# Kernel tuning notes

Hardware: AMD Instinct MI355X
Metric: run time of the kernel (lower is better)

Reference implementation:

```python
import jax, jax.numpy as jnp
import numpy as np

B, S, D = 8, 1024, 1024
E, M, K = 8, 4096, 2
GROUP = 1024
CAP = int(np.ceil(GROUP * K / E))  # 256 tokens per expert per group


def setup_inputs() -> dict:
    key = jax.random.key(0)
    ks = jax.random.split(key, 4)
    x = jax.random.normal(ks[0], (B, S, D), dtype=jnp.float32)
    w_router = jax.random.normal(ks[1], (D, E), dtype=jnp.float32) * 0.02
    w1 = jax.random.normal(ks[2], (E, D, M), dtype=jnp.float32) * (1.0 / np.sqrt(D))
    b1 = jnp.zeros((E, M), dtype=jnp.float32)
    w2 = jax.random.normal(ks[3], (E, M, D), dtype=jnp.float32) * (1.0 / np.sqrt(M))
    b2 = jnp.zeros((E, D), dtype=jnp.float32)
    return {"x": x, "w_router": w_router, "w1": w1, "b1": b1, "w2": w2, "b2": b2}


def _moe_forward(x, w_router, w1, b1, w2, b2):
    # Group tokens: [G, GROUP, D]
    xg = x.reshape(-1, GROUP, D)
    G = xg.shape[0]
    # Router: gates over experts per token.
    logits = jnp.einsum('gsd,de->gse', xg, w_router)
    gates = jax.nn.softmax(logits, axis=-1)  # [G, S, E]
    topk_vals, topk_idx = jax.lax.top_k(gates, K)  # [G, S, K]
    oh = jax.nn.one_hot(topk_idx, E, dtype=xg.dtype)  # [G, S, K, E]

    # Position in each expert's buffer: choice-0 of all tokens has priority
    # over choice-1 (standard top-k MoE priority ordering).
    prev = jnp.zeros((G, 1, E), dtype=xg.dtype)
    dispatch = jnp.zeros((G, GROUP, E, CAP), dtype=xg.dtype)
    combine = jnp.zeros((G, GROUP, E, CAP), dtype=xg.dtype)
    for k in range(K):
        ohk = oh[:, :, k, :]                                  # [G, S, E]
        csum = jnp.cumsum(ohk, axis=1) - ohk + prev           # slots used before this token
        pos_k = jnp.sum(csum * ohk, axis=-1)                  # [G, S]
        keep = (pos_k < CAP).astype(xg.dtype)
        pos_oh = jax.nn.one_hot(pos_k, CAP, dtype=xg.dtype)   # [G, S, C]
        d_k = ohk[:, :, :, None] * pos_oh[:, :, None, :] * keep[:, :, None, None]
        dispatch = dispatch + d_k
        combine = combine + topk_vals[:, :, k, None, None] * d_k
        prev = prev + jnp.sum(ohk, axis=1, keepdims=True)

    # Dispatch tokens into per-expert buffers: [E, G, C, D]
    xe = jnp.einsum('gsec,gsd->egcd', dispatch, xg)
    # Per-expert MLP (gelu, approximate=True as in flax Dense MlpBlock).
    h = jax.nn.gelu(jnp.einsum('egcd,edm->egcm', xe, w1) + b1[:, None, None, :])
    ye = jnp.einsum('egcm,emd->egcd', h, w2) + b2[:, None, None, :]
    # Combine back to tokens, weighted by gates.
    out = jnp.einsum('gsec,egcd->gsd', combine, ye)
    out = out.reshape(B, S, D)

    # Importance auxiliary metric (squared coefficient of variation of gate mass).
    imp = jnp.sum(gates, axis=1)  # [G, E]
    aux = jnp.mean((jnp.std(imp, axis=-1) / jnp.mean(imp, axis=-1)) ** 2)
    return out, aux


def reference(x, w_router, w1, b1, w2, b2):
    return _moe_forward(x, w_router, w1, b1, w2, b2)
```

## Files before the change

kernel.cpp:

```cpp
#include <hip/hip_runtime.h>

#define D_DIM 1024
#define E_EXP 8
#define M_DIM 4096
#define N_GRP 8
#define GRP_SZ 1024
#define CAPACITY 256
#define N_TOK (N_GRP * GRP_SZ)
#define SLOT_ROWS (E_EXP * N_GRP * CAPACITY)
#define ROWS_PER_E (N_GRP * CAPACITY)

typedef _Float16 half8_t __attribute__((ext_vector_type(8)));
typedef float f32x4_t __attribute__((ext_vector_type(4)));

__device__ __forceinline__ void async_copy16(void* lds, const void* gptr) {
  __builtin_amdgcn_global_load_lds(
      (__attribute__((address_space(1))) void*)(void*)(const_cast<void*>(gptr)),
      (__attribute__((address_space(3))) void*)lds,
      16, 0, 0);
}

__device__ __forceinline__ float fast_gelu(float v) {
  float w2 = 1.5957691216057308f * (v + 0.044715f * v * v * v);
  float ex = __expf(w2);
  float t = 1.0f - 2.0f * __builtin_amdgcn_rcpf(1.0f + ex);
  return 0.5f * v * (1.0f + t);
}

__global__ __launch_bounds__(256)
void router_kernel(const float* __restrict__ x, const float* __restrict__ wr,
                   float* __restrict__ gates, int* __restrict__ tk_idx,
                   float* __restrict__ tk_val) {
  __shared__ __attribute__((aligned(16))) float wrT[E_EXP * D_DIM];
  const int tid = threadIdx.x;
  for (int i = tid; i < E_EXP * D_DIM; i += 256) {
    int d = i >> 3, e = i & 7;
    wrT[e * D_DIM + d] = wr[i];
  }
  __syncthreads();
  const int wv = tid >> 6, lane = tid & 63;
  const int token = blockIdx.x * 4 + wv;
  const float4* xr = (const float4*)(x + (size_t)token * D_DIM);
  float lg[8] = {0.f, 0.f, 0.f, 0.f, 0.f, 0.f, 0.f, 0.f};
#pragma unroll
  for (int it = 0; it < 4; it++) {
    float4 v = xr[it * 64 + lane];
#pragma unroll
    for (int e = 0; e < 8; e++) {
      float4 w = *(const float4*)&wrT[e * D_DIM + (it * 64 + lane) * 4];
      lg[e] += v.x * w.x + v.y * w.y + v.z * w.z + v.w * w.w;
    }
  }
#pragma unroll
  for (int off = 32; off > 0; off >>= 1) {
#pragma unroll
    for (int e = 0; e < 8; e++) lg[e] += __shfl_xor(lg[e], off, 64);
  }
  if (lane == 0) {
    float mx = lg[0];
#pragma unroll
    for (int e = 1; e < 8; e++) mx = fmaxf(mx, lg[e]);
    float s = 0.f, g[8];
#pragma unroll
    for (int e = 0; e < 8; e++) { g[e] = expf(lg[e] - mx); s += g[e]; }
    float inv = 1.0f / s;
#pragma unroll
    for (int e = 0; e < 8; e++) { g[e] *= inv; gates[(size_t)token * 8 + e] = g[e]; }
    int i0 = 0; float v0 = g[0];
    for (int e = 1; e < 8; e++) if (g[e] > v0) { v0 = g[e]; i0 = e; }
    int i1 = -1; float v1 = -1.f;
    for (int e = 0; e < 8; e++) if (e != i0 && g[e] > v1) { v1 = g[e]; i1 = e; }
    tk_idx[token * 2 + 0] = i0; tk_idx[token * 2 + 1] = i1;
    tk_val[token * 2 + 0] = v0; tk_val[token * 2 + 1] = v1;
  }
}

__global__ void scan_kernel(const int* __restrict__ tk_idx,
                            int* __restrict__ slot_src,
                            int* __restrict__ assign_row) {
  const int g = blockIdx.x;
  const int lane = threadIdx.x;
  const unsigned long long below = (1ull << lane) - 1ull;
  int ev[32];
#pragma unroll
  for (int k = 0; k < 2; k++)
#pragma unroll
    for (int ch = 0; ch < 16; ch++)
      ev[k * 16 + ch] = tk_idx[((size_t)g * GRP_SZ + ch * 64 + lane) * 2 + k];
  int cnt[8] = {0, 0, 0, 0, 0, 0, 0, 0};
#pragma unroll
  for (int k = 0; k < 2; k++) {
#pragma unroll
    for (int ch = 0; ch < 16; ch++) {
      const int s = ch * 64 + lane;
      const int e = ev[k * 16 + ch];
      int pos = 0;
#pragma unroll
      for (int ee = 0; ee < 8; ee++) {
        unsigned long long m = __ballot(e == ee);
        if (e == ee) pos = cnt[ee] + (int)__popcll(m & below);
        cnt[ee] += (int)__popcll(m);
      }
      int row = (pos < CAPACITY) ? ((e * N_GRP + g) * CAPACITY + pos) : -1;
      assign_row[((size_t)g * GRP_SZ + s) * 2 + k] = row;
      if (row >= 0) slot_src[row] = s;
    }
  }
  for (int e = 0; e < 8; e++)
    for (int c = lane; c < CAPACITY; c += 64)
      if (c >= cnt[e]) slot_src[(e * N_GRP + g) * CAPACITY + c] = -1;
}

__global__ __launch_bounds__(256)
void gather_kernel(const float* __restrict__ x, const int* __restrict__ slot_src,
                   _Float16* __restrict__ A1) {
  const int row = blockIdx.x;
  const int g = (row >> 8) & 7;
  const int t = threadIdx.x;
  const int s = slot_src[row];
  float2* dst = (float2*)(A1 + (size_t)row * D_DIM);
  if (s < 0) { dst[t] = make_float2(0.f, 0.f); return; }
  const float4 v = ((const float4*)x)[((size_t)g * GRP_SZ + s) * (D_DIM / 4) + t];
  union { _Float16 h[4]; float2 f2; } u;
  u.h[0] = (_Float16)v.x; u.h[1] = (_Float16)v.y;
  u.h[2] = (_Float16)v.z; u.h[3] = (_Float16)v.w;
  dst[t] = u.f2;
}

__global__ __launch_bounds__(256)
void transpose_both_kernel(const float* __restrict__ w1, const float* __restrict__ w2,
                           _Float16* __restrict__ w1t, _Float16* __restrict__ w2t) {
  __shared__ float tile[32][33];
  const int z = blockIdx.y;
  const float* sp;
  _Float16* dp;
  int R, C;
  if (z < 8) { sp = w1 + (size_t)z * D_DIM * M_DIM; dp = w1t + (size_t)z * D_DIM * M_DIM; R = D_DIM; C = M_DIM; }
  else       { sp = w2 + (size_t)(z - 8) * M_DIM * D_DIM; dp = w2t + (size_t)(z - 8) * M_DIM * D_DIM; R = M_DIM; C = D_DIM; }
  const int tiles_x = C >> 5;
  const int c0 = (blockIdx.x % tiles_x) * 32, r0 = (blockIdx.x / tiles_x) * 32;
  {
    const int row = threadIdx.x >> 3;
    const int cb = (threadIdx.x & 7) * 4;
    float4 v = *(const float4*)&sp[(size_t)(r0 + row) * C + c0 + cb];
    tile[row][cb + 0] = v.x; tile[row][cb + 1] = v.y;
    tile[row][cb + 2] = v.z; tile[row][cb + 3] = v.w;
  }
  __syncthreads();
  const int cl = threadIdx.x >> 3;
  const int ch = threadIdx.x & 7;
  union { _Float16 h[4]; float2 f2; } u;
#pragma unroll
  for (int k = 0; k < 4; k++) u.h[k] = (_Float16)tile[ch * 4 + k][cl];
  *(float2*)&dp[(size_t)(c0 + cl) * R + r0 + ch * 4] = u.f2;
}

template <int KDIM, int NDIM, int EPI>
__global__ __launch_bounds__(256)
void gemm_bt_kernel(const _Float16* __restrict__ Aall,
                    const _Float16* __restrict__ BTall,
                    const float* __restrict__ biasAll,
                    void* __restrict__ CoutAll) {
  const int e = blockIdx.z;
  const _Float16* A = Aall + (size_t)e * ROWS_PER_E * KDIM;
  const _Float16* BT = BTall + (size_t)e * NDIM * KDIM;
  const float* bias = biasAll + (size_t)e * NDIM;

  constexpr int NYT = NDIM / 128;
  const int yt = blockIdx.x % NYT;
  const int xt = blockIdx.x / NYT;
  const int rowblk = xt * 128;
  const int colblk = yt * 128;

  const int tid = threadIdx.x;
  const int wave = tid >> 6, lane = tid & 63;
  const int wm = (wave & 1) * 64, wn = (wave >> 1) * 64;

  __shared__ __attribute__((aligned(16))) _Float16 As0[128 * 64];
  __shared__ __attribute__((aligned(16))) _Float16 As1[128 * 64];
  __shared__ __attribute__((aligned(16))) _Float16 Bs0[128 * 64];
  __shared__ __attribute__((aligned(16))) _Float16 Bs1[128 * 64];

  f32x4_t acc[4][4] = {};

  const int l_r = lane >> 3, l_c = lane & 7;
  const _Float16* gA[4];
  const _Float16* gB[4];
  int ldsOff[4];
#pragma unroll
  for (int i = 0; i < 4; i++) {
    const int rbase = i * 32 + wave * 8;
    const int r = rbase + l_r;
    const int q = l_c ^ (r & 7);
    gA[i] = A + (size_t)(rowblk + r) * KDIM + q * 8;
    gB[i] = BT + (size_t)(colblk + r) * KDIM + q * 8;
    ldsOff[i] = rbase * 64;
  }

  const int quad = lane >> 4;
  const int ln = lane & 15;
  int offA[4], offB[4];
#pragma unroll
  for (int i = 0; i < 4; i++) {
    int m = wm + i * 16 + ln;
    offA[i] = m * 64 + (quad ^ (m & 7)) * 8;
    int n = wn + i * 16 + ln;
    offB[i] = n * 64 + (quad ^ (n & 7)) * 8;
  }

  _Float16* curA = As0; _Float16* nxtA = As1;
  _Float16* curB = Bs0; _Float16* nxtB = Bs1;

#pragma unroll
  for (int i = 0; i < 4; i++) async_copy16(curA + ldsOff[i], gA[i]);
#pragma unroll
  for (int i = 0; i < 4; i++) async_copy16(curB + ldsOff[i], gB[i]);

  for (int kt = 0; kt < KDIM; kt += 64) {
    __syncthreads();
    if (kt + 64 < KDIM) {
#pragma unroll
      for (int i = 0; i < 4; i++) async_copy16(nxtA + ldsOff[i], gA[i] + kt + 64);
#pragma unroll
      for (int i = 0; i < 4; i++) async_copy16(nxtB + ldsOff[i], gB[i] + kt + 64);
    }
#pragma unroll
    for (int h = 0; h < 2; h++) {
      half8_t af[4], bf[4];
#pragma unroll
      for (int i = 0; i < 4; i++) {
        af[i] = *(const half8_t*)&curA[offA[i] ^ (h * 32)];
        bf[i] = *(const half8_t*)&curB[offB[i] ^ (h * 32)];
      }
#pragma unroll
      for (int i = 0; i < 4; i++)
#pragma unroll
        for (int j = 0; j < 4; j++)
          acc[i][j] = __builtin_amdgcn_mfma_f32_16x16x32_f16(af[i], bf[j], acc[i][j], 0, 0, 0);
    }
    _Float16* t;
    t = curA; curA = nxtA; nxtA = t;
    t = curB; curB = nxtB; nxtB = t;
  }

  if constexpr (EPI == 1) {
    _Float16* C = (_Float16*)CoutAll + (size_t)e * ROWS_PER_E * NDIM;
#pragma unroll
    for (int p = 0; p < 4; p++) {
      __syncthreads();
      const int lr0 = (wave & 1) * 16 + quad * 4;
#pragma unroll
      for (int j = 0; j < 4; j++) {
        const int col = wn + j * 16 + ln;
        const float bcol = bias[colblk + col];
#pragma unroll
        for (int r = 0; r < 4; r++) {
          float v = acc[p][j][r] + bcol;
          As0[(lr0 + r) * 136 + col] = (_Float16)fast_gelu(v);
        }
      }
      __syncthreads();
#pragma unroll
      for (int q = 0; q < 2; q++) {
        const int lrw = q * 16 + (tid >> 4);
        const int chunk = tid & 15;
        const int gr = (lrw >= 16 ? 64 : 0) + p * 16 + (lrw & 15);
        float4 vv = *(const float4*)&As0[lrw * 136 + chunk * 8];
        *(float4*)&C[(size_t)(rowblk + gr) * NDIM + colblk + chunk * 8] = vv;
      }
    }
  } else {
    float* C = (float*)CoutAll + (size_t)e * ROWS_PER_E * NDIM;
    const int colb = colblk + wn + ln;
    const int rowb = rowblk + wm + quad * 4;
#pragma unroll
    for (int j = 0; j < 4; j++) {
      const int col = colb + j * 16;
      const float bcol = bias[col];
#pragma unroll
      for (int i = 0; i < 4; i++) {
#pragma unroll
        for (int r = 0; r < 4; r++) {
          const int row = rowb + i * 16 + r;
          C[(size_t)row * NDIM + col] = acc[i][j][r] + bcol;
        }
      }
    }
  }
}

__global__ __launch_bounds__(256)
void combine_kernel(const float* __restrict__ ye, const int* __restrict__ assign_row,
                    const float* __restrict__ tk_val, float* __restrict__ out) {
  const int t = blockIdx.x;
  const int d = threadIdx.x;
  const int r0 = assign_row[t * 2 + 0];
  const int r1 = assign_row[t * 2 + 1];
  const float g0 = tk_val[t * 2 + 0];
  const float g1 = tk_val[t * 2 + 1];
  const float4* y4 = (const float4*)ye;
  float4 v = make_float4(0.f, 0.f, 0.f, 0.f);
  if (r0 >= 0) {
    float4 a = y4[(size_t)r0 * (D_DIM / 4) + d];
    v.x += g0 * a.x; v.y += g0 * a.y; v.z += g0 * a.z; v.w += g0 * a.w;
  }
  if (r1 >= 0) {
    float4 a = y4[(size_t)r1 * (D_DIM / 4) + d];
    v.x += g1 * a.x; v.y += g1 * a.y; v.z += g1 * a.z; v.w += g1 * a.w;
  }
  ((float4*)out)[(size_t)t * (D_DIM / 4) + d] = v;
}

__global__ __launch_bounds__(256)
void aux1_kernel(const float* __restrict__ gates, float* __restrict__ imp) {
  const int g = blockIdx.x >> 3, e = blockIdx.x & 7;
  const int tid = threadIdx.x, lane = tid & 63, wave = tid >> 6;
  float s = 0.f;
  for (int t = tid; t < GRP_SZ; t += 256)
    s += gates[((size_t)g * GRP_SZ + t) * 8 + e];
#pragma unroll
  for (int off = 32; off > 0; off >>= 1) s += __shfl_xor(s, off, 64);
  __shared__ float ws4[4];
  if (lane == 0) ws4[wave] = s;
  __syncthreads();
  if (tid == 0) imp[blockIdx.x] = ws4[0] + ws4[1] + ws4[2] + ws4[3];
}

__global__ void aux2_kernel(const float* __restrict__ imp, float* __restrict__ aux_out) {
  const int t = threadIdx.x;
  __shared__ float cvS[8];
  if (t < 8) {
    float mean = 0.f;
    for (int k = 0; k < 8; k++) mean += imp[t * 8 + k];
    mean *= 0.125f;
    float var = 0.f;
    for (int k = 0; k < 8; k++) { float dd = imp[t * 8 + k] - mean; var += dd * dd; }
    var *= 0.125f;
    cvS[t] = var / (mean * mean);
  }
  __syncthreads();
  if (t == 0) {
    float a = 0.f;
    for (int k = 0; k < 8; k++) a += cvS[k];
    aux_out[0] = a * 0.125f;
  }
}

extern "C" void kernel_launch(void* const* d_in, const int* in_sizes, int n_in,
                              void* d_out, int out_size, void* d_ws, size_t ws_size,
                              hipStream_t stream) {
  const float* x  = (const float*)d_in[0];
  const float* wr = (const float*)d_in[1];
  const float* w1 = (const float*)d_in[2];
  const float* b1 = (const float*)d_in[3];
  const float* w2 = (const float*)d_in[4];
  const float* b2 = (const float*)d_in[5];
  float* out = (float*)d_out;

  char* ws = (char*)d_ws;
  size_t off = 0;
  auto alloc = [&](size_t bytes) -> void* {
    void* p = ws + off;
    off += (bytes + 255) & ~(size_t)255;
    return p;
  };
  float*     gates      = (float*)alloc((size_t)N_TOK * 8 * 4);
  int*       tk_idx     = (int*)  alloc((size_t)N_TOK * 2 * 4);
  float*     tk_val     = (float*)alloc((size_t)N_TOK * 2 * 4);
  int*       assign_row = (int*)  alloc((size_t)N_TOK * 2 * 4);
  int*       slot_src   = (int*)  alloc((size_t)SLOT_ROWS * 4);
  float*     imp        = (float*)alloc(64 * 4);
  _Float16*  A1  = (_Float16*)alloc((size_t)SLOT_ROWS * D_DIM * 2);
  _Float16*  w1t = (_Float16*)alloc((size_t)E_EXP * M_DIM * D_DIM * 2);
  _Float16*  w2t = (_Float16*)alloc((size_t)E_EXP * D_DIM * M_DIM * 2);
  _Float16*  H   = (_Float16*)alloc((size_t)SLOT_ROWS * M_DIM * 2);
  float*     ye  = (float*)   alloc((size_t)SLOT_ROWS * D_DIM * 4);
  if (off > ws_size) return;

  router_kernel<<<N_TOK / 4, 256, 0, stream>>>(x, wr, gates, tk_idx, tk_val);
  scan_kernel<<<N_GRP, 64, 0, stream>>>(tk_idx, slot_src, assign_row);
  gather_kernel<<<SLOT_ROWS, 256, 0, stream>>>(x, slot_src, A1);
  transpose_both_kernel<<<dim3(4096, 16), 256, 0, stream>>>(w1, w2, w1t, w2t);
  gemm_bt_kernel<D_DIM, M_DIM, 1><<<dim3((ROWS_PER_E / 128) * (M_DIM / 128), 1, E_EXP), 256, 0, stream>>>(A1, w1t, b1, H);
  gemm_bt_kernel<M_DIM, D_DIM, 2><<<dim3((ROWS_PER_E / 128) * (D_DIM / 128), 1, E_EXP), 256, 0, stream>>>(H, w2t, b2, ye);
  combine_kernel<<<N_TOK, 256, 0, stream>>>(ye, assign_row, tk_val, out);
  aux1_kernel<<<64, 256, 0, stream>>>(gates, imp);
  aux2_kernel<<<1, 64, 0, stream>>>(imp, out + (size_t)N_TOK * D_DIM);
}
```

Before: 747.2 us.

## Replace expert GEMMs with 256x256-tile, 512-thread pipelined MFMA kernel

Rewrites the two per-expert GEMMs to use 256x256 output tiles with 8 waves, each wave computing a 128x64 sub-tile. The new kernel streams K in 32-wide sub-stages through a 128KB double-buffered LDS ring, waits on explicit vmcnt counts, and raises wave priority around MFMA bursts. Block indices are remapped for L2 locality. The goal is more operand reuse per LDS byte and better overlap of global loads with MFMA. In exchange, the dynamic LDS use is large and occupancy drops, the grid has fewer blocks (which may underfill CUs for the second GEMM), and the fragile wait counting raises correctness risk.

```diff
diff --git a/kernel.cpp b/kernel.cpp
--- a/kernel.cpp
+++ b/kernel.cpp
@@ -156,136 +156,153 @@
 }
 
 template <int KDIM, int NDIM, int EPI>
-__global__ __launch_bounds__(256)
-void gemm_bt_kernel(const _Float16* __restrict__ Aall,
+__global__ __launch_bounds__(512, 2)
+void gemm256_kernel(const _Float16* __restrict__ Aall,
                     const _Float16* __restrict__ BTall,
                     const float* __restrict__ biasAll,
                     void* __restrict__ CoutAll) {
+  constexpr int NT = KDIM / 64;
+  constexpr int NXT = ROWS_PER_E / 256;
+  constexpr int NYT = NDIM / 256;
+  constexpr int NB = NXT * NYT;
+  static_assert(NXT == 8 && (NB % 8) == 0 && NT >= 4, "geometry");
+
+  extern __shared__ __attribute__((aligned(16))) _Float16 smem[];
+  _Float16* lA = smem;
+  _Float16* lB = smem + 32768;
+
   const int e = blockIdx.z;
-  const _Float16* A = Aall + (size_t)e * ROWS_PER_E * KDIM;
+  const _Float16* A  = Aall  + (size_t)e * ROWS_PER_E * KDIM;
   const _Float16* BT = BTall + (size_t)e * NDIM * KDIM;
-  const float* bias = biasAll + (size_t)e * NDIM;
-
-  constexpr int NYT = NDIM / 128;
-  const int yt = blockIdx.x % NYT;
-  const int xt = blockIdx.x / NYT;
-  const int rowblk = xt * 128;
-  const int colblk = yt * 128;
+  const float* bias  = biasAll + (size_t)e * NDIM;
+
+  const int bswz = (blockIdx.x & 7) * (NB >> 3) + (blockIdx.x >> 3);
+  const int xt = bswz & (NXT - 1);
+  const int yt = bswz >> 3;
+  const int rowblk = xt * 256;
+  const int colblk = yt * 256;
 
   const int tid = threadIdx.x;
   const int wave = tid >> 6, lane = tid & 63;
-  const int wm = (wave & 1) * 64, wn = (wave >> 1) * 64;
-
-  __shared__ __attribute__((aligned(16))) _Float16 As0[128 * 64];
-  __shared__ __attribute__((aligned(16))) _Float16 As1[128 * 64];
-  __shared__ __attribute__((aligned(16))) _Float16 Bs0[128 * 64];
-  __shared__ __attribute__((aligned(16))) _Float16 Bs1[128 * 64];
-
-  f32x4_t acc[4][4] = {};
-
-  const int l_r = lane >> 3, l_c = lane & 7;
-  const _Float16* gA[4];
-  const _Float16* gB[4];
-  int ldsOff[4];
-#pragma unroll
-  for (int i = 0; i < 4; i++) {
-    const int rbase = i * 32 + wave * 8;
-    const int r = rbase + l_r;
-    const int q = l_c ^ (r & 7);
-    gA[i] = A + (size_t)(rowblk + r) * KDIM + q * 8;
-    gB[i] = BT + (size_t)(colblk + r) * KDIM + q * 8;
-    ldsOff[i] = rbase * 64;
-  }
-
-  const int quad = lane >> 4;
-  const int ln = lane & 15;
-  int offA[4], offB[4];
-#pragma unroll
-  for (int i = 0; i < 4; i++) {
-    int m = wm + i * 16 + ln;
-    offA[i] = m * 64 + (quad ^ (m & 7)) * 8;
-    int n = wn + i * 16 + ln;
-    offB[i] = n * 64 + (quad ^ (n & 7)) * 8;
-  }
-
-  _Float16* curA = As0; _Float16* nxtA = As1;
-  _Float16* curB = Bs0; _Float16* nxtB = Bs1;
-
-#pragma unroll
-  for (int i = 0; i < 4; i++) async_copy16(curA + ldsOff[i], gA[i]);
-#pragma unroll
-  for (int i = 0; i < 4; i++) async_copy16(curB + ldsOff[i], gB[i]);
-
-  for (int kt = 0; kt < KDIM; kt += 64) {
-    __syncthreads();
-    if (kt + 64 < KDIM) {
-#pragma unroll
-      for (int i = 0; i < 4; i++) async_copy16(nxtA + ldsOff[i], gA[i] + kt + 64);
-#pragma unroll
-      for (int i = 0; i < 4; i++) async_copy16(nxtB + ldsOff[i], gB[i] + kt + 64);
+  const int wm = wave >> 2, wn = wave & 3;
+  const int quad = lane >> 4, ln = lane & 15;
+
+  const int schunk = (tid & 7) ^ ((tid >> 3) & 7);
+  const int rowA = ((tid >> 3) << 1) + (schunk >> 2);
+  const int colA = (schunk & 3) << 3;
+  const _Float16* baseA = A  + (size_t)(rowblk + rowA) * KDIM + colA;
+  const _Float16* baseB = BT + (size_t)(colblk + rowA) * KDIM + colA;
+  const int ldsW = wave * 512;
+
+  auto stage_unit = [&](int u) {
+    const int tu = u >> 2;
+    const int j = u & 3;
+    const int ks = j >> 1;
+    const int koff = tu * 64 + ks * 32;
+    const int slot = ((tu & 1) * 2 + ks) * 8192 + ldsW;
+    if ((j & 1) == 0) {
+      const _Float16* g = baseA + koff;
+      async_copy16(lA + slot, g);
+      async_copy16(lA + slot + 4096, g + (size_t)128 * KDIM);
+    } else {
+      const _Float16* g = baseB + koff;
+      async_copy16(lB + slot, g);
+      async_copy16(lB + slot + 4096, g + (size_t)128 * KDIM);
     }
-#pragma unroll
-    for (int h = 0; h < 2; h++) {
-      half8_t af[4], bf[4];
-#pragma unroll
-      for (int i = 0; i < 4; i++) {
-        af[i] = *(const half8_t*)&curA[offA[i] ^ (h * 32)];
-        bf[i] = *(const half8_t*)&curB[offB[i] ^ (h * 32)];
+  };
+
+  const int swc = (((ln & 1) << 2) | quad) ^ (ln >> 1);
+  int offA[8], offB[4];
+#pragma unroll
+  for (int i = 0; i < 8; ++i)
+    offA[i] = (wm * 64 + i * 8 + (ln >> 1)) * 64 + swc * 8;
+#pragma unroll
+  for (int j = 0; j < 4; ++j)
+    offB[j] = (wn * 32 + j * 8 + (ln >> 1)) * 64 + swc * 8;
+
+  f32x4_t acc[8][4] = {};
+
+#pragma unroll
+  for (int u = 0; u < 5; ++u) stage_unit(u);
+  asm volatile("s_waitcnt vmcnt(6)" ::: "memory");
+  __builtin_amdgcn_s_barrier();
+
+  for (int t = 0; t < NT; ++t) {
+    const int bufo = (t & 1) * 2 * 8192;
+    half8_t bf[4];
+#pragma unroll
+    for (int p = 0; p < 4; ++p) {
+      const int ks = p >> 1;
+      const int ms = (p & 1) * 4;
+      const _Float16* Ap = lA + bufo + ks * 8192;
+      const _Float16* Bp = lB + bufo + ks * 8192;
+      half8_t af[4];
+#pragma unroll
+      for (int i = 0; i < 4; ++i) af[i] = *(const half8_t*)&Ap[offA[ms + i]];
+      if ((p & 1) == 0) {
+#pragma unroll
+        for (int j = 0; j < 4; ++j) bf[j] = *(const half8_t*)&Bp[offB[j]];
       }
-#pragma unroll
-      for (int i = 0; i < 4; i++)
-#pragma unroll
-        for (int j = 0; j < 4; j++)
-          acc[i][j] = __builtin_amdgcn_mfma_f32_16x16x32_f16(af[i], bf[j], acc[i][j], 0, 0, 0);
+      {
+        const int u = 4 * t + p + 5;
+        if (u < 4 * NT) stage_unit(u);
+      }
+      __builtin_amdgcn_s_barrier();
+      __builtin_amdgcn_s_setprio(1);
+#pragma unroll
+      for (int i = 0; i < 4; ++i)
+#pragma unroll
+        for (int j = 0; j < 4; ++j)
+          acc[ms + i][j] = __builtin_amdgcn_mfma_f32_16x16x32_f16(
+              af[i], bf[j], acc[ms + i][j], 0, 0, 0);
+      __builtin_amdgcn_s_setprio(0);
+      if (p == 1) {
+        if (t == NT - 1) asm volatile("s_waitcnt vmcnt(0)" ::: "memory");
+        else             asm volatile("s_waitcnt vmcnt(6)" ::: "memory");
+      } else if (p == 3) {
+        if (t == NT - 2)     asm volatile("s_waitcnt vmcnt(4)" ::: "memory");
+        else if (t < NT - 2) asm volatile("s_waitcnt vmcnt(6)" ::: "memory");
+      }
+      __builtin_amdgcn_s_barrier();
     }
-    _Float16* t;
-    t = curA; curA = nxtA; nxtA = t;
-    t = curB; curB = nxtB; nxtB = t;
-  }
+  }
+
+  __syncthreads();
+
+  float bcol[4];
+#pragma unroll
+  for (int j = 0; j < 4; ++j) bcol[j] = bias[colblk + wn * 64 + j * 16 + ln];
 
   if constexpr (EPI == 1) {
-    _Float16* C = (_Float16*)CoutAll + (size_t)e * ROWS_PER_E * NDIM;
-#pragma unroll
-    for (int p = 0; p < 4; p++) {
-      __syncthreads();
-      const int lr0 = (wave & 1) * 16 + quad * 4;
-#pragma unroll
-      for (int j = 0; j < 4; j++) {
-        const int col = wn + j * 16 + ln;
-        const float bcol = bias[colblk + col];
-#pragma unroll
-        for (int r = 0; r < 4; r++) {
-          float v = acc[p][j][r] + bcol;
-          As0[(lr0 + r) * 136 + col] = (_Float16)fast_gelu(v);
-        }
-      }
-      __syncthreads();
-#pragma unroll
-      for (int q = 0; q < 2; q++) {
-        const int lrw = q * 16 + (tid >> 4);
-        const int chunk = tid & 15;
-        const int gr = (lrw >= 16 ? 64 : 0) + p * 16 + (lrw & 15);
-        float4 vv = *(const float4*)&As0[lrw * 136 + chunk * 8];
-        *(float4*)&C[(size_t)(rowblk + gr) * NDIM + colblk + chunk * 8] = vv;
+    _Float16* Cc = (_Float16*)CoutAll + (size_t)e * ROWS_PER_E * NDIM;
+    _Float16* eb = smem + wave * 1280;
+#pragma unroll
+    for (int i = 0; i < 8; ++i) {
+#pragma unroll
+      for (int j = 0; j < 4; ++j)
+#pragma unroll
+        for (int r = 0; r < 4; ++r)
+          eb[(quad * 4 + r) * 72 + j * 16 + ln] =
+              (_Float16)fast_gelu(acc[i][j][r] + bcol[j]);
+#pragma unroll
+      for (int q = 0; q < 2; ++q) {
+        const int rl = q * 8 + (lane >> 3);
+        const int ch = lane & 7;
+        float4 vv = *(const float4*)&eb[rl * 72 + ch * 8];
+        *(float4*)&Cc[(size_t)(rowblk + wm * 128 + i * 16 + rl) * NDIM +
+                      colblk + wn * 64 + ch * 8] = vv;
       }
     }
   } else {
-    float* C = (float*)CoutAll + (size_t)e * ROWS_PER_E * NDIM;
-    const int colb = colblk + wn + ln;
-    const int rowb = rowblk + wm + quad * 4;
-#pragma unroll
-    for (int j = 0; j < 4; j++) {
-      const int col = colb + j * 16;
-      const float bcol = bias[col];
-#pragma unroll
-      for (int i = 0; i < 4; i++) {
-#pragma unroll
-        for (int r = 0; r < 4; r++) {
-          const int row = rowb + i * 16 + r;
-          C[(size_t)row * NDIM + col] = acc[i][j][r] + bcol;
-        }
-      }
-    }
+    float* Cc = (float*)CoutAll + (size_t)e * ROWS_PER_E * NDIM;
+#pragma unroll
+    for (int i = 0; i < 8; ++i)
+#pragma unroll
+      for (int j = 0; j < 4; ++j)
+#pragma unroll
+        for (int r = 0; r < 4; ++r)
+          Cc[(size_t)(rowblk + wm * 128 + i * 16 + quad * 4 + r) * NDIM +
+             colblk + wn * 64 + j * 16 + ln] = acc[i][j][r] + bcol[j];
   }
 }
 
@@ -381,8 +398,10 @@
   scan_kernel<<<N_GRP, 64, 0, stream>>>(tk_idx, slot_src, assign_row);
   gather_kernel<<<SLOT_ROWS, 256, 0, stream>>>(x, slot_src, A1);
   transpose_both_kernel<<<dim3(4096, 16), 256, 0, stream>>>(w1, w2, w1t, w2t);
-  gemm_bt_kernel<D_DIM, M_DIM, 1><<<dim3((ROWS_PER_E / 128) * (M_DIM / 128), 1, E_EXP), 256, 0, stream>>>(A1, w1t, b1, H);
-  gemm_bt_kernel<M_DIM, D_DIM, 2><<<dim3((ROWS_PER_E / 128) * (D_DIM / 128), 1, E_EXP), 256, 0, stream>>>(H, w2t, b2, ye);
+  gemm256_kernel<D_DIM, M_DIM, 1>
+      <<<dim3((ROWS_PER_E / 256) * (M_DIM / 256), 1, E_EXP), 512, 131072, stream>>>(A1, w1t, b1, H);
+  gemm256_kernel<M_DIM, D_DIM, 2>
+      <<<dim3((ROWS_PER_E / 256) * (D_DIM / 256), 1, E_EXP), 512, 131072, stream>>>(H, w2t, b2, ye);
   combine_kernel<<<N_TOK, 256, 0, stream>>>(ye, assign_row, tk_val, out);
   aux1_kernel<<<64, 256, 0, stream>>>(gates, imp);
   aux2_kernel<<<1, 64, 0, stream>>>(imp, out + (size_t)N_TOK * D_DIM);
```

Result: faster. 680.6 us (-8.9%).
